# Optimization experiments

Measured on AMD Instinct MI355X. Metric: run time of the kernel, lower is better.

## Reference

```python
import jax, jax.numpy as jnp
import numpy as np

CAPACITY_FACTOR = 1.0
MIN_CAPACITY = 4


def setup_inputs() -> dict:
    key = jax.random.key(0)
    ks = jax.random.split(key, 4)
    B, S, D, E, F = 4, 2048, 1024, 16, 4096
    hidden_states = jax.random.normal(ks[0], (B, S, D), dtype=jnp.float32)
    wg = jax.random.normal(ks[1], (D, E), dtype=jnp.float32) * 0.02
    w1 = jax.random.normal(ks[2], (E, D, F), dtype=jnp.float32) * (1.0 / np.sqrt(D))
    b1 = jnp.zeros((E, F), dtype=jnp.float32)
    w2 = jax.random.normal(ks[3], (E, F, D), dtype=jnp.float32) * (1.0 / np.sqrt(F))
    b2 = jnp.zeros((E, D), dtype=jnp.float32)
    return {"hidden_states": hidden_states, "wg": wg, "w1": w1, "b1": b1, "w2": w2, "b2": b2}


def reference(hidden_states, wg, w1, b1, w2, b2):
    B, S, D = hidden_states.shape
    x = hidden_states.reshape(-1, D)                      # [T, D] tokens
    T = x.shape[0]
    E = wg.shape[1]
    capacity = max(int(np.ceil(T / E * CAPACITY_FACTOR)), MIN_CAPACITY)  # static

    # ---- TopKGate (k=1, no noise, no RTS) ----
    logits = x @ wg                                       # [T, E]
    gates = jax.nn.softmax(logits, axis=-1)
    idx1 = jnp.argmax(gates, axis=1)                      # [T]
    mask1 = jax.nn.one_hot(idx1, E, dtype=gates.dtype)    # [T, E]
    exp_counts = jnp.sum(mask1, axis=0).astype(jnp.int32) # per-expert token counts

    # load-balancing aux loss
    me = jnp.mean(gates, axis=0)
    ce = jnp.mean(mask1, axis=0)
    l_aux = jnp.sum(me * ce) * E

    # slot assignment within each expert, drop overflow tokens
    locations1 = jnp.cumsum(mask1, axis=0) - 1.0          # [T, E]
    mask1 = mask1 * (locations1 < capacity).astype(gates.dtype)
    locations1_s = jnp.sum(locations1 * mask1, axis=1).astype(jnp.int32)  # [T]
    gates1 = gates * mask1                                # [T, E] gate prob of kept assignment

    loc_oh = jax.nn.one_hot(locations1_s, capacity, dtype=gates.dtype)    # [T, C]
    combine = jnp.einsum('te,tc->tec', gates1, loc_oh)    # [T, E, C]
    dispatch = (combine > 0).astype(x.dtype)              # [T, E, C]

    # ---- dispatch -> grouped expert FFN -> combine ----
    disp = jnp.einsum('tec,td->ecd', dispatch, x)         # [E, C, D]
    h = jax.nn.gelu(jnp.einsum('ecd,edf->ecf', disp, w1) + b1[:, None, :])
    eo = jnp.einsum('ecf,efd->ecd', h, w2) + b2[:, None, :]  # [E, C, D]
    out = jnp.einsum('tec,ecd->td', combine, eo).reshape(B, S, D)
    return out, l_aux, exp_counts
```

## Files before the change

### kernel.cpp

```cpp
#include <hip/hip_runtime.h>

typedef unsigned short u16;
typedef unsigned int   u32;
typedef unsigned long long u64;
typedef __attribute__((ext_vector_type(8))) __bf16 bf16x8;
typedef __attribute__((ext_vector_type(4))) float  f32x4;

#define TOK 8192
#define DIM 1024
#define NE  16
#define NF  4096
#define CAP 512

__device__ __forceinline__ u16 f2bf(float f) {
    u32 u = __float_as_uint(f);
    u32 r = (u + 0x7FFFu + ((u >> 16) & 1u)) >> 16;
    return (u16)r;
}

__device__ __forceinline__ float gelu_tanh(float x) {
    float u = 0.7978845608028654f * (x + 0.044715f * x * x * x);
    float t = __expf(-2.f * fabsf(u));
    float th = (1.f - t) / (1.f + t);
    th = (u < 0.f) ? -th : th;
    return 0.5f * x * (1.f + th);
}

__device__ __forceinline__ void gld16(const void* g, void* l) {
    __builtin_amdgcn_global_load_lds(
        (const __attribute__((address_space(1))) void*)g,
        (__attribute__((address_space(3))) void*)l, 16, 0, 0);
}

__global__ void moe_init(float* me_sums) {
    if (threadIdx.x < NE) me_sums[threadIdx.x] = 0.f;
}

__global__ void moe_wgT(const float* __restrict__ wg, float* __restrict__ wgT) {
    int i = blockIdx.x * 256 + threadIdx.x;
    int d = i >> 4, e = i & 15;
    wgT[(size_t)e * DIM + d] = wg[i];
}

__global__ void moe_gate(const float* __restrict__ x, const float* __restrict__ wgT,
                         int* __restrict__ eidx, float* __restrict__ gp,
                         float* __restrict__ me_sums) {
    __shared__ float lme[NE];
    const int tid = threadIdx.x;
    if (tid < NE) lme[tid] = 0.f;
    __syncthreads();
    const int tok = blockIdx.x * 16 + (tid >> 4);
    const int e   = tid & 15;
    const float4* xp = (const float4*)(x + (size_t)tok * DIM);
    const float4* wp = (const float4*)(wgT + (size_t)e * DIM);
    float acc = 0.f;
#pragma unroll 4
    for (int i = 0; i < DIM / 4; ++i) {
        float4 a = xp[i], b = wp[i];
        acc = fmaf(a.x, b.x, acc); acc = fmaf(a.y, b.y, acc);
        acc = fmaf(a.z, b.z, acc); acc = fmaf(a.w, b.w, acc);
    }
    float mx = acc;
    for (int off = 8; off; off >>= 1) mx = fmaxf(mx, __shfl_xor(mx, off, 16));
    float ex = __expf(acc - mx);
    float sum = ex;
    for (int off = 8; off; off >>= 1) sum += __shfl_xor(sum, off, 16);
    float p = ex / sum;
    atomicAdd(&lme[e], p);
    float bv = acc; int bi = e;
    for (int off = 8; off; off >>= 1) {
        float ov = __shfl_xor(bv, off, 16);
        int   oi = __shfl_xor(bi, off, 16);
        if (ov > bv || (ov == bv && oi < bi)) { bv = ov; bi = oi; }
    }
    float pw = __shfl(p, bi, 16);
    if (e == 0) { eidx[tok] = bi; gp[tok] = pw; }
    __syncthreads();
    if (tid < 16) atomicAdd(&me_sums[tid], lme[tid]);
}

__global__ void moe_scan(const int* __restrict__ eidx, const float* __restrict__ me_sums,
                         int* __restrict__ slot, int* __restrict__ tos,
                         float* __restrict__ tail ) {
    __shared__ int wcnt[16][16];
    __shared__ int base[16];
    const int tid = threadIdx.x, wid = tid >> 6, lane = tid & 63;
    if (tid < 16) base[tid] = 0;
    for (int i = tid; i < NE * CAP; i += 1024) tos[i] = -1;
    __syncthreads();
    const u64 below = ((u64)1 << lane) - 1;
    for (int chunk = 0; chunk < TOK / 1024; ++chunk) {
        int t = chunk * 1024 + tid;
        int e = eidx[t];
        int rank = 0;
#pragma unroll
        for (int ex = 0; ex < 16; ++ex) {
            u64 m = __ballot(e == ex);
            if (e == ex)    rank = __popcll(m & below);
            if (lane == ex) wcnt[wid][ex] = __popcll(m);
        }
        __syncthreads();
        int pre = base[e];
        for (int w = 0; w < wid; ++w) pre += wcnt[w][e];
        int s = pre + rank;
        slot[t] = s;
        if (s < CAP) tos[e * CAP + s] = t;
        __syncthreads();
        if (tid < 16) {
            int tot = 0;
            for (int w = 0; w < 16; ++w) tot += wcnt[w][tid];
            base[tid] += tot;
        }
        __syncthreads();
    }
    if (tid == 0) {
        float laux = 0.f;
        for (int e2 = 0; e2 < 16; ++e2) {
            float me = me_sums[e2] / (float)TOK;
            float ce = (float)base[e2] / (float)TOK;
            laux += me * ce;
        }
        tail[0] = laux * (float)NE;
    }
    if (tid < 16) tail[1 + tid] = (float)base[tid];
}

__global__ void moe_gather(const float* __restrict__ x, const int* __restrict__ tos,
                           u16* __restrict__ Xg) {
    const int s = blockIdx.x, tid = threadIdx.x;
    const int t = tos[s];
    float4 v = make_float4(0.f, 0.f, 0.f, 0.f);
    if (t >= 0) v = *(const float4*)(x + (size_t)t * DIM + tid * 4);
    u32 lo = (u32)f2bf(v.x) | ((u32)f2bf(v.y) << 16);
    u32 hi = (u32)f2bf(v.z) | ((u32)f2bf(v.w) << 16);
    *(uint2*)(Xg + (size_t)s * DIM + tid * 4) = make_uint2(lo, hi);
}

__global__ void moe_zero_dropped(const int* __restrict__ slot, float* __restrict__ out) {
    const int t = blockIdx.x;
    if (slot[t] < CAP) return;
    *(float4*)(out + (size_t)t * DIM + threadIdx.x * 4) = make_float4(0.f, 0.f, 0.f, 0.f);
}

__global__ void moe_convT(const float* __restrict__ src, u16* __restrict__ dst,
                          int R, int C) {
    __shared__ float tile[64][65];
    int b = blockIdx.x;
    const int tilesC = C >> 6, tilesR = R >> 6;
    int tc = b % tilesC; b /= tilesC;
    int tr = b % tilesR; int e = b / tilesR;
    const float* S = src + ((size_t)e * R + tr * 64) * C + tc * 64;
    const int tid = threadIdx.x;
    const int rr = tid >> 4, cc = (tid & 15) * 4;
#pragma unroll
    for (int i = 0; i < 4; ++i) {
        float4 v = *(const float4*)(S + (size_t)(rr + i * 16) * C + cc);
        tile[rr + i * 16][cc + 0] = v.x; tile[rr + i * 16][cc + 1] = v.y;
        tile[rr + i * 16][cc + 2] = v.z; tile[rr + i * 16][cc + 3] = v.w;
    }
    __syncthreads();
    const int c = tid >> 2, r0 = (tid & 3) * 16;
    u16 tmp[16];
#pragma unroll
    for (int k = 0; k < 16; ++k) tmp[k] = f2bf(tile[r0 + k][c]);
    u16* D = dst + ((size_t)e * C + tc * 64 + c) * R + tr * 64 + r0;
    uint4 w0 = make_uint4((u32)tmp[0] | ((u32)tmp[1] << 16), (u32)tmp[2] | ((u32)tmp[3] << 16),
                          (u32)tmp[4] | ((u32)tmp[5] << 16), (u32)tmp[6] | ((u32)tmp[7] << 16));
    uint4 w1 = make_uint4((u32)tmp[8] | ((u32)tmp[9] << 16), (u32)tmp[10] | ((u32)tmp[11] << 16),
                          (u32)tmp[12] | ((u32)tmp[13] << 16), (u32)tmp[14] | ((u32)tmp[15] << 16));
    *(uint4*)(D) = w0;
    *(uint4*)(D + 8) = w1;
}

__global__ __launch_bounds__(256) void moe_gemm1(const u16* __restrict__ Xg,
                                                 const u16* __restrict__ W1t,
                                                 const float* __restrict__ b1,
                                                 u16* __restrict__ H) {
    __shared__ alignas(16) u16 Als[2][4096];
    __shared__ alignas(16) u16 Bls[2][4096];
    const int tid = threadIdx.x, wave = tid >> 6, lane = tid & 63;
    const int flat = blockIdx.x;
    const int xcd  = flat & 7;
    const int slot = flat >> 3;
    const int e    = xcd * 2 + (slot >> 7);
    const int tile = slot & 127;
    const int bmL  = tile & 3;
    const int bn   = tile >> 2;
    const int bm   = e * 4 + bmL;
    const int r4  = lane >> 2;
    const int gch = (lane & 3) ^ ((lane >> 3) & 3);
    const u16* aS = Xg + (size_t)(bm * 128 + wave * 32 + r4) * DIM + gch * 8;
    const u16* bS = W1t + (size_t)e * NF * DIM
                  + (size_t)(bn * 128 + wave * 32 + r4) * DIM + gch * 8;
    u16* aD0 = &Als[0][wave * 1024]; u16* aD1 = &Als[1][wave * 1024];
    u16* bD0 = &Bls[0][wave * 1024]; u16* bD1 = &Bls[1][wave * 1024];
    f32x4 acc[4][4] = {};
    const int wm = wave & 1, wn = wave >> 1;
    const int fr = lane & 15, fq = lane >> 4;
    const int rdoff = fr * 32 + (fq ^ ((fr >> 1) & 3)) * 8;

#define STAGE1(AD, BD, K) do { \
        gld16(aS + (K), AD); gld16(aS + (K) + 16 * DIM, (AD) + 512); \
        gld16(bS + (K), BD); gld16(bS + (K) + 16 * DIM, (BD) + 512); } while (0)
#define COMP1(AB, BB) do { \
        bf16x8 aF[4], bF[4]; \
        _Pragma("unroll") for (int i = 0; i < 4; ++i) \
            aF[i] = *(const bf16x8*)(const void*)((AB) + (wm * 64 + i * 16) * 32 + rdoff); \
        _Pragma("unroll") for (int j = 0; j < 4; ++j) \
            bF[j] = *(const bf16x8*)(const void*)((BB) + (wn * 64 + j * 16) * 32 + rdoff); \
        _Pragma("unroll") for (int i = 0; i < 4; ++i) \
        _Pragma("unroll") for (int j = 0; j < 4; ++j) \
            acc[i][j] = __builtin_amdgcn_mfma_f32_16x16x32_bf16(aF[i], bF[j], acc[i][j], 0, 0, 0); \
        } while (0)

    STAGE1(aD0, bD0, 0);
    for (int k0 = 0; k0 < DIM; k0 += 64) {
        __syncthreads();
        if (k0 + 32 < DIM) STAGE1(aD1, bD1, k0 + 32);
        COMP1(&Als[0][0], &Bls[0][0]);
        __syncthreads();
        if (k0 + 64 < DIM) STAGE1(aD0, bD0, k0 + 64);
        COMP1(&Als[1][0], &Bls[1][0]);
    }
#undef STAGE1
#undef COMP1

    const int mBase = bm * 128 + wm * 64;
    const int nBase = bn * 128 + wn * 64;
#pragma unroll
    for (int j = 0; j < 4; ++j) {
        const int f = nBase + j * 16 + fr;
        const float bias = b1[e * NF + f];
#pragma unroll
        for (int i = 0; i < 4; ++i) {
            const int m0 = mBase + i * 16 + fq * 4;
#pragma unroll
            for (int r = 0; r < 4; ++r) {
                float v = acc[i][j][r] + bias;
                H[(size_t)(m0 + r) * NF + f] = f2bf(gelu_tanh(v));
            }
        }
    }
}

__global__ __launch_bounds__(256) void moe_gemm2(const u16* __restrict__ H,
                                                 const u16* __restrict__ W2t,
                                                 const float* __restrict__ b2,
                                                 const int* __restrict__ tos,
                                                 const float* __restrict__ gp,
                                                 float* __restrict__ out) {
    __shared__ alignas(16) u16 Als[2][4096];
    __shared__ alignas(16) u16 Bls[2][4096];
    const int tid = threadIdx.x, wave = tid >> 6, lane = tid & 63;
    const int flat = blockIdx.x;
    const int xcd  = flat & 7;
    const int slot = flat >> 3;
    const int e    = xcd * 2 + (slot >> 5);
    const int tile = slot & 31;
    const int bmL  = tile & 3;
    const int bn   = tile >> 2;
    const int bm   = e * 4 + bmL;
    const int r4  = lane >> 2;
    const int gch = (lane & 3) ^ ((lane >> 3) & 3);
    const u16* aS = H + (size_t)(bm * 128 + wave * 32 + r4) * NF + gch * 8;
    const u16* bS = W2t + (size_t)e * DIM * NF
                  + (size_t)(bn * 128 + wave * 32 + r4) * NF + gch * 8;
    u16* aD0 = &Als[0][wave * 1024]; u16* aD1 = &Als[1][wave * 1024];
    u16* bD0 = &Bls[0][wave * 1024]; u16* bD1 = &Bls[1][wave * 1024];
    f32x4 acc[4][4] = {};
    const int wm = wave & 1, wn = wave >> 1;
    const int fr = lane & 15, fq = lane >> 4;
    const int rdoff = fr * 32 + (fq ^ ((fr >> 1) & 3)) * 8;

#define STAGE2(AD, BD, K) do { \
        gld16(aS + (K), AD); gld16(aS + (K) + 16 * NF, (AD) + 512); \
        gld16(bS + (K), BD); gld16(bS + (K) + 16 * NF, (BD) + 512); } while (0)
#define COMP2(AB, BB) do { \
        bf16x8 aF[4], bF[4]; \
        _Pragma("unroll") for (int i = 0; i < 4; ++i) \
            aF[i] = *(const bf16x8*)(const void*)((AB) + (wm * 64 + i * 16) * 32 + rdoff); \
        _Pragma("unroll") for (int j = 0; j < 4; ++j) \
            bF[j] = *(const bf16x8*)(const void*)((BB) + (wn * 64 + j * 16) * 32 + rdoff); \
        _Pragma("unroll") for (int i = 0; i < 4; ++i) \
        _Pragma("unroll") for (int j = 0; j < 4; ++j) \
            acc[i][j] = __builtin_amdgcn_mfma_f32_16x16x32_bf16(aF[i], bF[j], acc[i][j], 0, 0, 0); \
        } while (0)

    STAGE2(aD0, bD0, 0);
    for (int k0 = 0; k0 < NF; k0 += 64) {
        __syncthreads();
        if (k0 + 32 < NF) STAGE2(aD1, bD1, k0 + 32);
        COMP2(&Als[0][0], &Bls[0][0]);
        __syncthreads();
        if (k0 + 64 < NF) STAGE2(aD0, bD0, k0 + 64);
        COMP2(&Als[1][0], &Bls[1][0]);
    }
#undef STAGE2
#undef COMP2

    const int mBase = bm * 128 + wm * 64;
    const int nBase = bn * 128 + wn * 64;
#pragma unroll
    for (int i = 0; i < 4; ++i) {
#pragma unroll
        for (int r = 0; r < 4; ++r) {
            const int m = mBase + i * 16 + fq * 4 + r;
            const int t = tos[m];
            if (t < 0) continue;
            const float g = gp[t];
#pragma unroll
            for (int j = 0; j < 4; ++j) {
                const int d = nBase + j * 16 + fr;
                out[(size_t)t * DIM + d] = g * (acc[i][j][r] + b2[e * DIM + d]);
            }
        }
    }
}

extern "C" void kernel_launch(void* const* d_in, const int* in_sizes, int n_in,
                              void* d_out, int out_size, void* d_ws, size_t ws_size,
                              hipStream_t stream) {
    const float* x  = (const float*)d_in[0];
    const float* wg = (const float*)d_in[1];
    const float* w1 = (const float*)d_in[2];
    const float* b1 = (const float*)d_in[3];
    const float* w2 = (const float*)d_in[4];
    const float* b2 = (const float*)d_in[5];
    float* out = (float*)d_out;

    char* ws = (char*)d_ws;
    const size_t WBF_OFF = 0;
    const size_t XG_OFF  = WBF_OFF + (size_t)NE * NF * DIM * 2;
    const size_t H_OFF   = XG_OFF + (size_t)TOK * DIM * 2;
    const size_t SM_OFF  = H_OFF + (size_t)TOK * NF * 2;
    u16* Wbf = (u16*)(ws + WBF_OFF);
    u16* Xg  = (u16*)(ws + XG_OFF);
    u16* H   = (u16*)(ws + H_OFF);
    int*   eidx = (int*)(ws + SM_OFF);
    float* gp   = (float*)(ws + SM_OFF + 32768);
    int*   slot = (int*)(ws + SM_OFF + 65536);
    int*   tos  = (int*)(ws + SM_OFF + 98304);
    float* me   = (float*)(ws + SM_OFF + 131072);
    float* wgT  = (float*)(ws + SM_OFF + 131072 + 128);

    float* tail = out + (size_t)TOK * DIM;

    moe_init<<<1, 64, 0, stream>>>(me);
    moe_wgT<<<64, 256, 0, stream>>>(wg, wgT);
    moe_gate<<<TOK / 16, 256, 0, stream>>>(x, wgT, eidx, gp, me);
    moe_scan<<<1, 1024, 0, stream>>>(eidx, me, slot, tos, tail);
    moe_gather<<<NE * CAP, 256, 0, stream>>>(x, tos, Xg);
    moe_zero_dropped<<<TOK, 256, 0, stream>>>(slot, out);
    moe_convT<<<NE * (DIM / 64) * (NF / 64), 256, 0, stream>>>(w1, Wbf, DIM, NF);
    moe_gemm1<<<2048, 256, 0, stream>>>(Xg, Wbf, b1, H);
    moe_convT<<<NE * (NF / 64) * (DIM / 64), 256, 0, stream>>>(w2, Wbf, NF, DIM);
    moe_gemm2<<<512, 256, 0, stream>>>(H, Wbf, b2, tos, gp, out);
}
```

Measured before the change: 932.4 us.

## Enlarge GEMM tiles to 256x256 with 8 waves and triple-buffered LDS pipeline

Both expert GEMMs move from 128x128 tiles with 4 waves and a double-buffered LDS loop to larger tiles (256x256 for gemm1, 256x128 for gemm2) with 8 waves per block. Loads use a 3-stage ring with explicit vmcnt waits and a single barrier per k-step, plus raised wave priority around the MFMA bursts. The aim is better data reuse per global byte and deeper overlap of loads with matrix math. In exchange each block needs more LDS and registers, and the grids shrink to 512 and 256 blocks, which may leave fewer blocks per CU to hide latency.

```diff
diff --git a/kernel.cpp b/kernel.cpp
--- a/kernel.cpp
+++ b/kernel.cpp
@@ -172,149 +172,204 @@
     *(uint4*)(D + 8) = w1;
 }
 
-__global__ __launch_bounds__(256) void moe_gemm1(const u16* __restrict__ Xg,
-                                                 const u16* __restrict__ W1t,
-                                                 const float* __restrict__ b1,
-                                                 u16* __restrict__ H) {
-    __shared__ alignas(16) u16 Als[2][4096];
-    __shared__ alignas(16) u16 Bls[2][4096];
-    const int tid = threadIdx.x, wave = tid >> 6, lane = tid & 63;
-    const int flat = blockIdx.x;
-    const int xcd  = flat & 7;
-    const int slot = flat >> 3;
-    const int e    = xcd * 2 + (slot >> 7);
-    const int tile = slot & 127;
-    const int bmL  = tile & 3;
-    const int bn   = tile >> 2;
-    const int bm   = e * 4 + bmL;
-    const int r4  = lane >> 2;
-    const int gch = (lane & 3) ^ ((lane >> 3) & 3);
-    const u16* aS = Xg + (size_t)(bm * 128 + wave * 32 + r4) * DIM + gch * 8;
-    const u16* bS = W1t + (size_t)e * NF * DIM
-                  + (size_t)(bn * 128 + wave * 32 + r4) * DIM + gch * 8;
-    u16* aD0 = &Als[0][wave * 1024]; u16* aD1 = &Als[1][wave * 1024];
-    u16* bD0 = &Bls[0][wave * 1024]; u16* bD1 = &Bls[1][wave * 1024];
-    f32x4 acc[4][4] = {};
-    const int wm = wave & 1, wn = wave >> 1;
-    const int fr = lane & 15, fq = lane >> 4;
-    const int rdoff = fr * 32 + (fq ^ ((fr >> 1) & 3)) * 8;
-
-#define STAGE1(AD, BD, K) do { \
-        gld16(aS + (K), AD); gld16(aS + (K) + 16 * DIM, (AD) + 512); \
-        gld16(bS + (K), BD); gld16(bS + (K) + 16 * DIM, (BD) + 512); } while (0)
-#define COMP1(AB, BB) do { \
-        bf16x8 aF[4], bF[4]; \
-        _Pragma("unroll") for (int i = 0; i < 4; ++i) \
-            aF[i] = *(const bf16x8*)(const void*)((AB) + (wm * 64 + i * 16) * 32 + rdoff); \
-        _Pragma("unroll") for (int j = 0; j < 4; ++j) \
-            bF[j] = *(const bf16x8*)(const void*)((BB) + (wn * 64 + j * 16) * 32 + rdoff); \
-        _Pragma("unroll") for (int i = 0; i < 4; ++i) \
-        _Pragma("unroll") for (int j = 0; j < 4; ++j) \
-            acc[i][j] = __builtin_amdgcn_mfma_f32_16x16x32_bf16(aF[i], bF[j], acc[i][j], 0, 0, 0); \
-        } while (0)
-
-    STAGE1(aD0, bD0, 0);
-    for (int k0 = 0; k0 < DIM; k0 += 64) {
-        __syncthreads();
-        if (k0 + 32 < DIM) STAGE1(aD1, bD1, k0 + 32);
-        COMP1(&Als[0][0], &Bls[0][0]);
-        __syncthreads();
-        if (k0 + 64 < DIM) STAGE1(aD0, bD0, k0 + 64);
-        COMP1(&Als[1][0], &Bls[1][0]);
-    }
-#undef STAGE1
-#undef COMP1
-
-    const int mBase = bm * 128 + wm * 64;
-    const int nBase = bn * 128 + wn * 64;
-#pragma unroll
-    for (int j = 0; j < 4; ++j) {
-        const int f = nBase + j * 16 + fr;
-        const float bias = b1[e * NF + f];
-#pragma unroll
-        for (int i = 0; i < 4; ++i) {
-            const int m0 = mBase + i * 16 + fq * 4;
-#pragma unroll
-            for (int r = 0; r < 4; ++r) {
-                float v = acc[i][j][r] + bias;
-                H[(size_t)(m0 + r) * NF + f] = f2bf(gelu_tanh(v));
-            }
-        }
-    }
-}
-
-__global__ __launch_bounds__(256) void moe_gemm2(const u16* __restrict__ H,
-                                                 const u16* __restrict__ W2t,
-                                                 const float* __restrict__ b2,
-                                                 const int* __restrict__ tos,
-                                                 const float* __restrict__ gp,
-                                                 float* __restrict__ out) {
-    __shared__ alignas(16) u16 Als[2][4096];
-    __shared__ alignas(16) u16 Bls[2][4096];
+__global__ __launch_bounds__(512, 2) void moe_gemm1(const u16* __restrict__ Xg,
+                                                    const u16* __restrict__ W1t,
+                                                    const float* __restrict__ b1,
+                                                    u16* __restrict__ H) {
+    __shared__ alignas(16) u16 Als[3][8192];
+    __shared__ alignas(16) u16 Bls[3][8192];
     const int tid = threadIdx.x, wave = tid >> 6, lane = tid & 63;
     const int flat = blockIdx.x;
     const int xcd  = flat & 7;
     const int slot = flat >> 3;
     const int e    = xcd * 2 + (slot >> 5);
     const int tile = slot & 31;
-    const int bmL  = tile & 3;
-    const int bn   = tile >> 2;
-    const int bm   = e * 4 + bmL;
-    const int r4  = lane >> 2;
-    const int gch = (lane & 3) ^ ((lane >> 3) & 3);
-    const u16* aS = H + (size_t)(bm * 128 + wave * 32 + r4) * NF + gch * 8;
-    const u16* bS = W2t + (size_t)e * DIM * NF
-                  + (size_t)(bn * 128 + wave * 32 + r4) * NF + gch * 8;
-    u16* aD0 = &Als[0][wave * 1024]; u16* aD1 = &Als[1][wave * 1024];
-    u16* bD0 = &Bls[0][wave * 1024]; u16* bD1 = &Bls[1][wave * 1024];
-    f32x4 acc[4][4] = {};
+    const int bm   = tile & 1;
+    const int bn   = tile >> 1;
+    const int r4   = lane >> 2;
+    const int gch  = (lane & 3) ^ ((lane >> 3) & 3);
+    const u16* aSrc = Xg + (size_t)(e * 512 + bm * 256 + wave * 16 + r4) * DIM + gch * 8;
+    const u16* bSrc = W1t + (size_t)e * NF * DIM
+                    + (size_t)(bn * 256 + wave * 16 + r4) * DIM + gch * 8;
     const int wm = wave & 1, wn = wave >> 1;
     const int fr = lane & 15, fq = lane >> 4;
     const int rdoff = fr * 32 + (fq ^ ((fr >> 1) & 3)) * 8;
 
-#define STAGE2(AD, BD, K) do { \
-        gld16(aS + (K), AD); gld16(aS + (K) + 16 * NF, (AD) + 512); \
-        gld16(bS + (K), BD); gld16(bS + (K) + 16 * NF, (BD) + 512); } while (0)
-#define COMP2(AB, BB) do { \
-        bf16x8 aF[4], bF[4]; \
-        _Pragma("unroll") for (int i = 0; i < 4; ++i) \
-            aF[i] = *(const bf16x8*)(const void*)((AB) + (wm * 64 + i * 16) * 32 + rdoff); \
-        _Pragma("unroll") for (int j = 0; j < 4; ++j) \
-            bF[j] = *(const bf16x8*)(const void*)((BB) + (wn * 64 + j * 16) * 32 + rdoff); \
-        _Pragma("unroll") for (int i = 0; i < 4; ++i) \
-        _Pragma("unroll") for (int j = 0; j < 4; ++j) \
-            acc[i][j] = __builtin_amdgcn_mfma_f32_16x16x32_bf16(aF[i], bF[j], acc[i][j], 0, 0, 0); \
-        } while (0)
-
-    STAGE2(aD0, bD0, 0);
-    for (int k0 = 0; k0 < NF; k0 += 64) {
-        __syncthreads();
-        if (k0 + 32 < NF) STAGE2(aD1, bD1, k0 + 32);
-        COMP2(&Als[0][0], &Bls[0][0]);
-        __syncthreads();
-        if (k0 + 64 < NF) STAGE2(aD0, bD0, k0 + 64);
-        COMP2(&Als[1][0], &Bls[1][0]);
+    f32x4 acc[2][4][4] = {};
+
+#define STAGE1(P, T) do { \
+        const int ko = (T) * 32; \
+        u16* ad = &Als[P][wave * 512]; \
+        u16* bd = &Bls[P][wave * 512]; \
+        gld16(aSrc + ko, ad); \
+        gld16(aSrc + 128 * DIM + ko, ad + 4096); \
+        gld16(bSrc + ko, bd); \
+        gld16(bSrc + 128 * DIM + ko, bd + 4096); } while (0)
+
+    const int NT = DIM / 32;
+    STAGE1(0, 0);
+    STAGE1(1, 1);
+    int c = 0;
+    for (int t = 0; t < NT; ++t) {
+        if (t < NT - 1) { asm volatile("s_waitcnt vmcnt(4)" ::: "memory"); }
+        else            { asm volatile("s_waitcnt vmcnt(0)" ::: "memory"); }
+        __builtin_amdgcn_sched_barrier(0);
+        __builtin_amdgcn_s_barrier();
+        __builtin_amdgcn_sched_barrier(0);
+        const u16* Ab = &Als[c][0];
+        const u16* Bb = &Bls[c][0];
+        bf16x8 bF[4], aF[4];
+#pragma unroll
+        for (int j = 0; j < 4; ++j)
+            bF[j] = *(const bf16x8*)(const void*)(Bb + (wn * 64 + j * 16) * 32 + rdoff);
+#pragma unroll
+        for (int i = 0; i < 4; ++i)
+            aF[i] = *(const bf16x8*)(const void*)(Ab + (wm * 128 + i * 16) * 32 + rdoff);
+        if (t + 2 < NT) {
+            const int p = (c + 2 >= 3) ? (c - 1) : (c + 2);
+            STAGE1(p, t + 2);
+        }
+        __builtin_amdgcn_sched_barrier(0);
+        __builtin_amdgcn_s_setprio(1);
+#pragma unroll
+        for (int i = 0; i < 4; ++i)
+#pragma unroll
+            for (int j = 0; j < 4; ++j)
+                acc[0][i][j] = __builtin_amdgcn_mfma_f32_16x16x32_bf16(aF[i], bF[j], acc[0][i][j], 0, 0, 0);
+        __builtin_amdgcn_s_setprio(0);
+#pragma unroll
+        for (int i = 0; i < 4; ++i)
+            aF[i] = *(const bf16x8*)(const void*)(Ab + (wm * 128 + 64 + i * 16) * 32 + rdoff);
+        __builtin_amdgcn_s_setprio(1);
+#pragma unroll
+        for (int i = 0; i < 4; ++i)
+#pragma unroll
+            for (int j = 0; j < 4; ++j)
+                acc[1][i][j] = __builtin_amdgcn_mfma_f32_16x16x32_bf16(aF[i], bF[j], acc[1][i][j], 0, 0, 0);
+        __builtin_amdgcn_s_setprio(0);
+        c = (c == 2) ? 0 : c + 1;
+    }
+#undef STAGE1
+
+    const int mBase = e * 512 + bm * 256 + wm * 128;
+    const int nBase = bn * 256 + wn * 64;
+#pragma unroll
+    for (int j = 0; j < 4; ++j) {
+        const int f = nBase + j * 16 + fr;
+        const float bias = b1[e * NF + f];
+#pragma unroll
+        for (int q = 0; q < 2; ++q)
+#pragma unroll
+            for (int i = 0; i < 4; ++i) {
+                const int m0 = mBase + q * 64 + i * 16 + fq * 4;
+#pragma unroll
+                for (int r = 0; r < 4; ++r) {
+                    float v = acc[q][i][j][r] + bias;
+                    H[(size_t)(m0 + r) * NF + f] = f2bf(gelu_tanh(v));
+                }
+            }
+    }
+}
+
+__global__ __launch_bounds__(512, 2) void moe_gemm2(const u16* __restrict__ H,
+                                                    const u16* __restrict__ W2t,
+                                                    const float* __restrict__ b2,
+                                                    const int* __restrict__ tos,
+                                                    const float* __restrict__ gp,
+                                                    float* __restrict__ out) {
+    __shared__ alignas(16) u16 Als[3][8192];
+    __shared__ alignas(16) u16 Bls[3][4096];
+    const int tid = threadIdx.x, wave = tid >> 6, lane = tid & 63;
+    const int flat = blockIdx.x;
+    const int xcd  = flat & 7;
+    const int slot = flat >> 3;
+    const int e    = xcd * 2 + (slot >> 4);
+    const int tile = slot & 15;
+    const int bm   = tile & 1;
+    const int bn   = tile >> 1;
+    const int r4   = lane >> 2;
+    const int gch  = (lane & 3) ^ ((lane >> 3) & 3);
+    const u16* aSrc = H + (size_t)(e * 512 + bm * 256 + wave * 16 + r4) * NF + gch * 8;
+    const u16* bSrc = W2t + (size_t)e * DIM * NF
+                    + (size_t)(bn * 128 + wave * 16 + r4) * NF + gch * 8;
+    const int wm = wave & 1, wn = wave >> 1;
+    const int fr = lane & 15, fq = lane >> 4;
+    const int rdoff = fr * 32 + (fq ^ ((fr >> 1) & 3)) * 8;
+
+    f32x4 acc[2][4][2] = {};
+
+#define STAGE2(P, T) do { \
+        const int ko = (T) * 32; \
+        u16* ad = &Als[P][wave * 512]; \
+        u16* bd = &Bls[P][wave * 512]; \
+        gld16(aSrc + ko, ad); \
+        gld16(aSrc + (size_t)128 * NF + ko, ad + 4096); \
+        gld16(bSrc + ko, bd); } while (0)
+
+    const int NT = NF / 32;
+    STAGE2(0, 0);
+    STAGE2(1, 1);
+    int c = 0;
+    for (int t = 0; t < NT; ++t) {
+        if (t < NT - 1) { asm volatile("s_waitcnt vmcnt(3)" ::: "memory"); }
+        else            { asm volatile("s_waitcnt vmcnt(0)" ::: "memory"); }
+        __builtin_amdgcn_sched_barrier(0);
+        __builtin_amdgcn_s_barrier();
+        __builtin_amdgcn_sched_barrier(0);
+        const u16* Ab = &Als[c][0];
+        const u16* Bb = &Bls[c][0];
+        bf16x8 bF[2], aF[4];
+#pragma unroll
+        for (int j = 0; j < 2; ++j)
+            bF[j] = *(const bf16x8*)(const void*)(Bb + (wn * 32 + j * 16) * 32 + rdoff);
+#pragma unroll
+        for (int i = 0; i < 4; ++i)
+            aF[i] = *(const bf16x8*)(const void*)(Ab + (wm * 128 + i * 16) * 32 + rdoff);
+        if (t + 2 < NT) {
+            const int p = (c + 2 >= 3) ? (c - 1) : (c + 2);
+            STAGE2(p, t + 2);
+        }
+        __builtin_amdgcn_sched_barrier(0);
+        __builtin_amdgcn_s_setprio(1);
+#pragma unroll
+        for (int i = 0; i < 4; ++i)
+#pragma unroll
+            for (int j = 0; j < 2; ++j)
+                acc[0][i][j] = __builtin_amdgcn_mfma_f32_16x16x32_bf16(aF[i], bF[j], acc[0][i][j], 0, 0, 0);
+        __builtin_amdgcn_s_setprio(0);
+#pragma unroll
+        for (int i = 0; i < 4; ++i)
+            aF[i] = *(const bf16x8*)(const void*)(Ab + (wm * 128 + 64 + i * 16) * 32 + rdoff);
+        __builtin_amdgcn_s_setprio(1);
+#pragma unroll
+        for (int i = 0; i < 4; ++i)
+#pragma unroll
+            for (int j = 0; j < 2; ++j)
+                acc[1][i][j] = __builtin_amdgcn_mfma_f32_16x16x32_bf16(aF[i], bF[j], acc[1][i][j], 0, 0, 0);
+        __builtin_amdgcn_s_setprio(0);
+        c = (c == 2) ? 0 : c + 1;
     }
 #undef STAGE2
-#undef COMP2
-
-    const int mBase = bm * 128 + wm * 64;
-    const int nBase = bn * 128 + wn * 64;
-#pragma unroll
-    for (int i = 0; i < 4; ++i) {
-#pragma unroll
-        for (int r = 0; r < 4; ++r) {
-            const int m = mBase + i * 16 + fq * 4 + r;
-            const int t = tos[m];
-            if (t < 0) continue;
-            const float g = gp[t];
-#pragma unroll
-            for (int j = 0; j < 4; ++j) {
-                const int d = nBase + j * 16 + fr;
-                out[(size_t)t * DIM + d] = g * (acc[i][j][r] + b2[e * DIM + d]);
+
+    const int mBase = e * 512 + bm * 256 + wm * 128;
+    const int nBase = bn * 128 + wn * 32;
+#pragma unroll
+    for (int q = 0; q < 2; ++q)
+#pragma unroll
+        for (int i = 0; i < 4; ++i) {
+#pragma unroll
+            for (int r = 0; r < 4; ++r) {
+                const int m = mBase + q * 64 + i * 16 + fq * 4 + r;
+                const int t = tos[m];
+                if (t < 0) continue;
+                const float g = gp[t];
+#pragma unroll
+                for (int j = 0; j < 2; ++j) {
+                    const int d = nBase + j * 16 + fr;
+                    out[(size_t)t * DIM + d] = g * (acc[q][i][j][r] + b2[e * DIM + d]);
+                }
             }
         }
-    }
 }
 
 extern "C" void kernel_launch(void* const* d_in, const int* in_sizes, int n_in,
@@ -352,7 +407,7 @@
     moe_gather<<<NE * CAP, 256, 0, stream>>>(x, tos, Xg);
     moe_zero_dropped<<<TOK, 256, 0, stream>>>(slot, out);
     moe_convT<<<NE * (DIM / 64) * (NF / 64), 256, 0, stream>>>(w1, Wbf, DIM, NF);
-    moe_gemm1<<<2048, 256, 0, stream>>>(Xg, Wbf, b1, H);
+    moe_gemm1<<<512, 512, 0, stream>>>(Xg, Wbf, b1, H);
     moe_convT<<<NE * (NF / 64) * (DIM / 64), 256, 0, stream>>>(w2, Wbf, NF, DIM);
-    moe_gemm2<<<512, 256, 0, stream>>>(H, Wbf, b2, tos, gp, out);
-}
+    moe_gemm2<<<256, 512, 0, stream>>>(H, Wbf, b2, tos, gp, out);
+}
```

After: 929.4 us. Within noise of the previous version (-0.3%).
